# Performance work log

Measured on AMD Instinct MI355X. Metric: run time of the kernel, lower is better.

Reference implementation:

```python
import jax, jax.numpy as jnp
import numpy as np

B, N, D, L = 32, 1024, 128, 2  # batch graphs, nodes, hidden dim, num GIN layers
BN_EPS = 1e-5


def _batchnorm(x2d, gamma, beta):
    # Training-mode BatchNorm1d over flattened (B*N, D) with biased variance
    mean = jnp.mean(x2d, axis=0)
    var = jnp.mean(jnp.square(x2d - mean), axis=0)
    return (x2d - mean) * (gamma / jnp.sqrt(var + BN_EPS)) + beta


def setup_inputs() -> dict:
    key = jax.random.key(0)
    ks = jax.random.split(key, 12)
    s = 1.0 / np.sqrt(D)  # torch Linear default init scale
    inp = {
        "x": jax.random.normal(ks[0], (B, N, D), dtype=jnp.float32),
        "padded_nei": jax.random.randint(ks[1], (B, N, 8), 0, N, dtype=jnp.int64),
        "adj": jax.random.uniform(ks[2], (B, N, N), dtype=jnp.float32),
        # stacked per-layer params [L, ...]
        "W1": jax.random.uniform(ks[3], (L, D, D), jnp.float32, -s, s),
        "b1": jax.random.uniform(ks[4], (L, D), jnp.float32, -s, s),
        "W2": jax.random.uniform(ks[5], (L, D, D), jnp.float32, -s, s),
        "b2": jax.random.uniform(ks[6], (L, D), jnp.float32, -s, s),
        "g_in": jnp.ones((L, D), jnp.float32),   # MLP-internal BN gamma
        "be_in": jnp.zeros((L, D), jnp.float32),  # MLP-internal BN beta
        "g_out": jnp.ones((L, D), jnp.float32),  # GraphCNN outer BN gamma
        "be_out": jnp.zeros((L, D), jnp.float32),
    }
    return inp


def reference(x, padded_nei, adj, W1, b1, W2, b2, g_in, be_in, g_out, be_out):
    h = x  # [B, N, D]
    for l in range(L):
        # sum-pooling over neighbors via batched dense adjacency matmul
        pooled = jnp.einsum('bij,bjd->bid', adj, h)  # [B, N, D]
        # MLP: Linear -> BN -> ReLU -> Linear
        z = pooled @ W1[l] + b1[l]
        z = jax.nn.relu(_batchnorm(z.reshape(-1, D), g_in[l], be_in[l])).reshape(B, N, D)
        z = z @ W2[l] + b2[l]
        # outer BatchNorm1d + ReLU
        h = jax.nn.relu(_batchnorm(z.reshape(-1, D), g_out[l], be_out[l])).reshape(B, N, D)
    return h
```

## Files before the change

### kernel.cpp

```cpp
#include <hip/hip_runtime.h>
#include <stdint.h>


#define BB 32
#define NN 1024
#define DD 128
#define RR 32768

typedef __bf16 bf16_t;
typedef bf16_t bf16x8 __attribute__((ext_vector_type(8)));
typedef float f32x4 __attribute__((ext_vector_type(4)));

__device__ __forceinline__ unsigned short f2b(float f) {
  unsigned u = __float_as_uint(f);
  u += 0x7fff + ((u >> 16) & 1);
  return (unsigned short)(u >> 16);
}
__device__ __forceinline__ float b2f(unsigned short s) {
  return __uint_as_float((unsigned)s << 16);
}

__global__ __launch_bounds__(256) void k0_prep(const float* __restrict__ x,
                                               const float* __restrict__ W1,
                                               const float* __restrict__ W2,
                                               unsigned short* __restrict__ hT,
                                               unsigned short* __restrict__ W1T,
                                               unsigned short* __restrict__ W2T) {
  const int tid = threadIdx.x;
  if (blockIdx.x < 256) {
    const int b = blockIdx.x >> 3, nt = blockIdx.x & 7;
    __shared__ alignas(16) unsigned short T[128][136];
    const int r = tid >> 1, c0 = (tid & 1) * 64;
    const float* src = x + ((size_t)(b * 8 + nt) * 128 + r) * 128 + c0;
#pragma unroll
    for (int i = 0; i < 64; i += 4) {
      float4 v = *(const float4*)(src + i);
      int c = c0 + i;
      T[c][r] = f2b(v.x); T[c + 1][r] = f2b(v.y);
      T[c + 2][r] = f2b(v.z); T[c + 3][r] = f2b(v.w);
    }
    __syncthreads();
    const int d = tid >> 1, n0 = (tid & 1) * 64;
    unsigned short* dst = hT + ((size_t)b * DD + d) * NN + nt * 128 + n0;
#pragma unroll
    for (int i = 0; i < 64; i += 8)
      *(uint4*)(dst + i) = *(const uint4*)&T[d][n0 + i];
  } else {
    int idx = (blockIdx.x - 256) * 256 + tid;
    int w = idx >> 15;
    int rem = idx & 32767;
    int l = rem >> 14;
    int n = (rem >> 7) & 127;
    int k = rem & 127;
    const float* W = w ? W2 : W1;
    unsigned short* WT = w ? W2T : W1T;
    WT[((size_t)l * 128 + n) * 128 + k] = f2b(W[((size_t)l * 128 + k) * 128 + n]);
  }
}

__global__ __launch_bounds__(256, 2) void kA_pool_lin(
    const float* __restrict__ adj, const unsigned short* __restrict__ hT,
    const unsigned short* __restrict__ WT, const float* __restrict__ bias,
    unsigned short* __restrict__ z1b, float* __restrict__ gsum,
    float* __restrict__ gsq) {
  const int mt = blockIdx.x, b = blockIdx.y;
  const int tid = threadIdx.x;
  const int wave = tid >> 6, lane = tid & 63;
  const int wc = wave * 32;
  const int ln = lane & 15, q = lane >> 4;

  __shared__ union {
    struct {
      alignas(16) unsigned short As[64][72];
      alignas(16) unsigned short Bs[128][72];
    } p1;
    alignas(16) unsigned short As2[64][136];
  } sm;
  __shared__ alignas(16) unsigned short Ws[128][136];

#pragma unroll
  for (int p = 0; p < 8; p++) {
    int c = tid + p * 256;
    int n = c >> 4, k8 = (c & 15) * 8;
    *(uint4*)&Ws[n][k8] = *(const uint4*)&WT[n * 128 + k8];
  }

  const float* adjb = adj + ((size_t)b * NN + mt * 64) * NN;
  const unsigned short* hTb = hT + (size_t)b * DD * NN;

  f32x4 acc1[4][2];
  f32x4 zero = {0.f, 0.f, 0.f, 0.f};
#pragma unroll
  for (int i = 0; i < 4; i++) { acc1[i][0] = zero; acc1[i][1] = zero; }

  const int ar = tid >> 2, aseg = (tid & 3) * 16;
  const int br = tid >> 1, bh = (tid & 1) * 32;
  const float* pAsrc = adjb + (size_t)ar * NN + aseg;
  const unsigned short* pBsrc = hTb + (size_t)br * NN + bh;

  float4 pa[4];
  uint4 pb[4];
#pragma unroll
  for (int u = 0; u < 4; u++) {
    pa[u] = *(const float4*)(pAsrc + u * 4);
    pb[u] = *(const uint4*)(pBsrc + u * 8);
  }

  for (int k0 = 0; k0 < NN; k0 += 64) {
    __syncthreads();
    {
      alignas(16) unsigned short t[16];
#pragma unroll
      for (int u = 0; u < 4; u++) {
        t[u * 4] = f2b(pa[u].x); t[u * 4 + 1] = f2b(pa[u].y);
        t[u * 4 + 2] = f2b(pa[u].z); t[u * 4 + 3] = f2b(pa[u].w);
      }
      *(uint4*)&sm.p1.As[ar][aseg] = *(const uint4*)&t[0];
      *(uint4*)&sm.p1.As[ar][aseg + 8] = *(const uint4*)&t[8];
#pragma unroll
      for (int u = 0; u < 4; u++) *(uint4*)&sm.p1.Bs[br][bh + u * 8] = pb[u];
    }
    __syncthreads();
    if (k0 + 64 < NN) {
#pragma unroll
      for (int u = 0; u < 4; u++) {
        pa[u] = *(const float4*)(pAsrc + k0 + 64 + u * 4);
        pb[u] = *(const uint4*)(pBsrc + k0 + 64 + u * 8);
      }
    }
#pragma unroll
    for (int kk = 0; kk < 2; kk++) {
      bf16x8 af[4], bfr[2];
#pragma unroll
      for (int i = 0; i < 4; i++)
        af[i] = *(const bf16x8*)&sm.p1.As[i * 16 + ln][kk * 32 + q * 8];
#pragma unroll
      for (int j = 0; j < 2; j++)
        bfr[j] = *(const bf16x8*)&sm.p1.Bs[wc + j * 16 + ln][kk * 32 + q * 8];
#pragma unroll
      for (int i = 0; i < 4; i++)
#pragma unroll
        for (int j = 0; j < 2; j++)
          acc1[i][j] = __builtin_amdgcn_mfma_f32_16x16x32_bf16(af[i], bfr[j], acc1[i][j], 0, 0, 0);
    }
  }

  __syncthreads();
#pragma unroll
  for (int i = 0; i < 4; i++) {
    int row = i * 16 + q * 4;
#pragma unroll
    for (int j = 0; j < 2; j++) {
      int col = wc + j * 16 + ln;
#pragma unroll
      for (int r = 0; r < 4; r++) sm.As2[row + r][col] = f2b(acc1[i][j][r]);
    }
  }
  __syncthreads();

  f32x4 acc2[4][2];
#pragma unroll
  for (int i = 0; i < 4; i++) { acc2[i][0] = zero; acc2[i][1] = zero; }
#pragma unroll
  for (int ks = 0; ks < 4; ks++) {
    bf16x8 af[4], bfr[2];
#pragma unroll
    for (int i = 0; i < 4; i++)
      af[i] = *(const bf16x8*)&sm.As2[i * 16 + ln][ks * 32 + q * 8];
#pragma unroll
    for (int j = 0; j < 2; j++)
      bfr[j] = *(const bf16x8*)&Ws[wc + j * 16 + ln][ks * 32 + q * 8];
#pragma unroll
    for (int i = 0; i < 4; i++)
#pragma unroll
      for (int j = 0; j < 2; j++)
        acc2[i][j] = __builtin_amdgcn_mfma_f32_16x16x32_bf16(af[i], bfr[j], acc2[i][j], 0, 0, 0);
  }

  const size_t row0 = (size_t)b * NN + mt * 64;
#pragma unroll
  for (int j = 0; j < 2; j++) {
    int col = wc + j * 16 + ln;
    float bc = bias[col];
    float s1 = 0.f, s2 = 0.f;
#pragma unroll
    for (int i = 0; i < 4; i++) {
      int row = i * 16 + q * 4;
#pragma unroll
      for (int r = 0; r < 4; r++) {
        float v = acc2[i][j][r] + bc;
        z1b[(row0 + row + r) * 128 + col] = f2b(v);
        s1 += v; s2 += v * v;
      }
    }
    s1 += __shfl_xor(s1, 16); s1 += __shfl_xor(s1, 32);
    s2 += __shfl_xor(s2, 16); s2 += __shfl_xor(s2, 32);
    if (q == 0) { atomicAdd(&gsum[col], s1); atomicAdd(&gsq[col], s2); }
  }
}

__global__ __launch_bounds__(256, 2) void kB_lin(
    const unsigned short* __restrict__ Zin, const float* __restrict__ gsum_in,
    const float* __restrict__ gsq_in, const float* __restrict__ gamma,
    const float* __restrict__ beta, const unsigned short* __restrict__ WT,
    const float* __restrict__ bias, unsigned short* __restrict__ z2b,
    float* __restrict__ gsum, float* __restrict__ gsq) {
  const int mt = blockIdx.x;
  const int tid = threadIdx.x;
  const int wave = tid >> 6, lane = tid & 63;
  const int wc = wave * 32;
  const int ln = lane & 15, q = lane >> 4;

  __shared__ alignas(16) unsigned short Az[64][136];
  __shared__ alignas(16) unsigned short Ws[128][136];
  __shared__ float nsc[128], nsh[128];

  if (tid < 128) {
    float mean = gsum_in[tid] * (1.f / 32768.f);
    float var = gsq_in[tid] * (1.f / 32768.f) - mean * mean;
    float sc = gamma[tid] * rsqrtf(var + 1e-5f);
    nsc[tid] = sc; nsh[tid] = beta[tid] - mean * sc;
  }
#pragma unroll
  for (int p = 0; p < 8; p++) {
    int c = tid + p * 256;
    int n = c >> 4, k8 = (c & 15) * 8;
    *(uint4*)&Ws[n][k8] = *(const uint4*)&WT[n * 128 + k8];
  }
  __syncthreads();

  const size_t row0 = (size_t)mt * 64;
  {
    const int r = tid >> 2, c0 = (tid & 3) * 32;
    const unsigned short* src = Zin + (row0 + r) * 128 + c0;
#pragma unroll
    for (int u = 0; u < 4; u++) {
      uint4 raw = *(const uint4*)(src + u * 8);
      const unsigned short* s = (const unsigned short*)&raw;
      alignas(16) unsigned short t[8];
#pragma unroll
      for (int e = 0; e < 8; e++) {
        int c = c0 + u * 8 + e;
        t[e] = f2b(fmaxf(fmaf(b2f(s[e]), nsc[c], nsh[c]), 0.f));
      }
      *(uint4*)&Az[r][c0 + u * 8] = *(const uint4*)&t[0];
    }
  }
  __syncthreads();

  f32x4 acc[4][2];
  f32x4 zero = {0.f, 0.f, 0.f, 0.f};
#pragma unroll
  for (int i = 0; i < 4; i++) { acc[i][0] = zero; acc[i][1] = zero; }
#pragma unroll
  for (int ks = 0; ks < 4; ks++) {
    bf16x8 af[4], bfr[2];
#pragma unroll
    for (int i = 0; i < 4; i++)
      af[i] = *(const bf16x8*)&Az[i * 16 + ln][ks * 32 + q * 8];
#pragma unroll
    for (int j = 0; j < 2; j++)
      bfr[j] = *(const bf16x8*)&Ws[wc + j * 16 + ln][ks * 32 + q * 8];
#pragma unroll
    for (int i = 0; i < 4; i++)
#pragma unroll
      for (int j = 0; j < 2; j++)
        acc[i][j] = __builtin_amdgcn_mfma_f32_16x16x32_bf16(af[i], bfr[j], acc[i][j], 0, 0, 0);
  }

#pragma unroll
  for (int j = 0; j < 2; j++) {
    int col = wc + j * 16 + ln;
    float bc = bias[col];
    float s1 = 0.f, s2 = 0.f;
#pragma unroll
    for (int i = 0; i < 4; i++) {
      int row = i * 16 + q * 4;
#pragma unroll
      for (int r = 0; r < 4; r++) {
        float v = acc[i][j][r] + bc;
        z2b[(row0 + row + r) * 128 + col] = f2b(v);
        s1 += v; s2 += v * v;
      }
    }
    s1 += __shfl_xor(s1, 16); s1 += __shfl_xor(s1, 32);
    s2 += __shfl_xor(s2, 16); s2 += __shfl_xor(s2, 32);
    if (q == 0) { atomicAdd(&gsum[col], s1); atomicAdd(&gsq[col], s2); }
  }
}

__global__ __launch_bounds__(256) void k4_bnt(const unsigned short* __restrict__ Z,
                                              const float* __restrict__ gsum,
                                              const float* __restrict__ gsq,
                                              const float* __restrict__ gamma,
                                              const float* __restrict__ beta,
                                              unsigned short* __restrict__ hT) {
  const int b = blockIdx.x, nt = blockIdx.y, tid = threadIdx.x;
  __shared__ alignas(16) unsigned short T[128][136];
  __shared__ float nsc[128], nsh[128];
  if (tid < 128) {
    float mean = gsum[tid] * (1.f / 32768.f);
    float var = gsq[tid] * (1.f / 32768.f) - mean * mean;
    float sc = gamma[tid] * rsqrtf(var + 1e-5f);
    nsc[tid] = sc; nsh[tid] = beta[tid] - mean * sc;
  }
  __syncthreads();
  const int r = tid >> 1, c0 = (tid & 1) * 64;
  const unsigned short* src = Z + ((size_t)(b * 8 + nt) * 128 + r) * 128 + c0;
#pragma unroll
  for (int u = 0; u < 8; u++) {
    uint4 raw = *(const uint4*)(src + u * 8);
    const unsigned short* s = (const unsigned short*)&raw;
#pragma unroll
    for (int e = 0; e < 8; e++) {
      int c = c0 + u * 8 + e;
      T[c][r] = f2b(fmaxf(fmaf(b2f(s[e]), nsc[c], nsh[c]), 0.f));
    }
  }
  __syncthreads();
  const int d = tid >> 1, n0 = (tid & 1) * 64;
  unsigned short* dst = hT + ((size_t)b * DD + d) * NN + nt * 128 + n0;
#pragma unroll
  for (int i = 0; i < 64; i += 8)
    *(uint4*)(dst + i) = *(const uint4*)&T[d][n0 + i];
}

__global__ __launch_bounds__(256) void k4_out(const unsigned short* __restrict__ Z,
                                              const float* __restrict__ gsum,
                                              const float* __restrict__ gsq,
                                              const float* __restrict__ gamma,
                                              const float* __restrict__ beta,
                                              float* __restrict__ out) {
  const int blk = blockIdx.x, tid = threadIdx.x;
  __shared__ float nsc[128], nsh[128];
  if (tid < 128) {
    float mean = gsum[tid] * (1.f / 32768.f);
    float var = gsq[tid] * (1.f / 32768.f) - mean * mean;
    float sc = gamma[tid] * rsqrtf(var + 1e-5f);
    nsc[tid] = sc; nsh[tid] = beta[tid] - mean * sc;
  }
  __syncthreads();
  const int r = tid >> 1, c0 = (tid & 1) * 64;
  const unsigned short* src = Z + ((size_t)blk * 128 + r) * 128 + c0;
  float* dst = out + ((size_t)blk * 128 + r) * 128 + c0;
#pragma unroll
  for (int u = 0; u < 8; u++) {
    uint4 raw = *(const uint4*)(src + u * 8);
    const unsigned short* s = (const unsigned short*)&raw;
    float4 o;
    int c = c0 + u * 8;
    o.x = fmaxf(fmaf(b2f(s[0]), nsc[c], nsh[c]), 0.f);
    o.y = fmaxf(fmaf(b2f(s[1]), nsc[c + 1], nsh[c + 1]), 0.f);
    o.z = fmaxf(fmaf(b2f(s[2]), nsc[c + 2], nsh[c + 2]), 0.f);
    o.w = fmaxf(fmaf(b2f(s[3]), nsc[c + 3], nsh[c + 3]), 0.f);
    *(float4*)(dst + u * 8) = o;
    o.x = fmaxf(fmaf(b2f(s[4]), nsc[c + 4], nsh[c + 4]), 0.f);
    o.y = fmaxf(fmaf(b2f(s[5]), nsc[c + 5], nsh[c + 5]), 0.f);
    o.z = fmaxf(fmaf(b2f(s[6]), nsc[c + 6], nsh[c + 6]), 0.f);
    o.w = fmaxf(fmaf(b2f(s[7]), nsc[c + 7], nsh[c + 7]), 0.f);
    *(float4*)(dst + u * 8 + 4) = o;
  }
}

extern "C" void kernel_launch(void* const* d_in, const int* in_sizes, int n_in,
                              void* d_out, int out_size, void* d_ws, size_t ws_size,
                              hipStream_t stream) {
  const float* x = (const float*)d_in[0];
  const float* adj = (const float*)d_in[2];
  const float* W1 = (const float*)d_in[3];
  const float* b1 = (const float*)d_in[4];
  const float* W2 = (const float*)d_in[5];
  const float* b2 = (const float*)d_in[6];
  const float* g_in = (const float*)d_in[7];
  const float* be_in = (const float*)d_in[8];
  const float* g_out = (const float*)d_in[9];
  const float* be_out = (const float*)d_in[10];
  float* out = (float*)d_out;

  char* ws = (char*)d_ws;
  unsigned short* hT = (unsigned short*)ws;
  unsigned short* z1b = (unsigned short*)(ws + 8ull * 1024 * 1024);
  unsigned short* z2b = (unsigned short*)(ws + 16ull * 1024 * 1024);
  unsigned short* W1T = (unsigned short*)(ws + 24ull * 1024 * 1024);
  unsigned short* W2T = W1T + 2 * 128 * 128;
  float* stats = (float*)(ws + 25ull * 1024 * 1024);

  hipMemsetAsync(stats, 0, 4 * 256 * sizeof(float), stream);
  k0_prep<<<512, 256, 0, stream>>>(x, W1, W2, hT, W1T, W2T);

  for (int l = 0; l < 2; l++) {
    float* st_in = stats + (l * 2 + 0) * 256;
    float* st_out = stats + (l * 2 + 1) * 256;
    kA_pool_lin<<<dim3(16, 32), 256, 0, stream>>>(adj, hT, W1T + l * 16384,
                                                  b1 + l * 128, z1b, st_in,
                                                  st_in + 128);
    kB_lin<<<512, 256, 0, stream>>>(z1b, st_in, st_in + 128, g_in + l * 128,
                                    be_in + l * 128, W2T + l * 16384,
                                    b2 + l * 128, z2b, st_out, st_out + 128);
    if (l == 0)
      k4_bnt<<<dim3(32, 8), 256, 0, stream>>>(z2b, st_out, st_out + 128, g_out,
                                              be_out, hT);
    else
      k4_out<<<256, 256, 0, stream>>>(z2b, st_out, st_out + 128, g_out + 128,
                                      be_out + 128, out);
  }
}
```

Baseline: 371.7 us.

## Pre-convert adjacency to bf16 and stream tiles into LDS asynchronously

The prep kernel gains extra blocks that convert the fp32 adjacency to a bf16 copy in workspace. The pooling kernel then reads that copy. Its main loop is replaced by a double-buffered pipeline that loads tiles straight into LDS with global_load_lds, using an XOR-swizzled layout to avoid bank conflicts and explicit vmcnt waits plus barriers. The second linear layer's weight fragments move from LDS into registers. This aims to hide global load latency and remove the per-thread fp32-to-bf16 conversion in the hot loop, at the cost of an extra conversion pass over adjacency, a large added workspace buffer, and higher register use.

```diff
diff --git a/kernel.cpp b/kernel.cpp
--- a/kernel.cpp
+++ b/kernel.cpp
@@ -20,13 +20,29 @@
   return __uint_as_float((unsigned)s << 16);
 }
 
+#define GLL(GP, LP)                                              \
+  __builtin_amdgcn_global_load_lds(                              \
+      (const __attribute__((address_space(1))) void*)(GP),       \
+      (__attribute__((address_space(3))) void*)(LP), 16, 0, 0)
+
 __global__ __launch_bounds__(256) void k0_prep(const float* __restrict__ x,
+                                               const float* __restrict__ adj,
                                                const float* __restrict__ W1,
                                                const float* __restrict__ W2,
                                                unsigned short* __restrict__ hT,
                                                unsigned short* __restrict__ W1T,
-                                               unsigned short* __restrict__ W2T) {
+                                               unsigned short* __restrict__ W2T,
+                                               unsigned short* __restrict__ adjB) {
   const int tid = threadIdx.x;
+  if (blockIdx.x >= 512) {
+    size_t i8 = ((size_t)(blockIdx.x - 512) * 256 + tid) * 8;
+    float4 a = *(const float4*)(adj + i8);
+    float4 b = *(const float4*)(adj + i8 + 4);
+    alignas(16) unsigned short t[8] = {f2b(a.x), f2b(a.y), f2b(a.z), f2b(a.w),
+                                       f2b(b.x), f2b(b.y), f2b(b.z), f2b(b.w)};
+    *(uint4*)(adjB + i8) = *(const uint4*)t;
+    return;
+  }
   if (blockIdx.x < 256) {
     const int b = blockIdx.x >> 3, nt = blockIdx.x & 7;
     __shared__ alignas(16) unsigned short T[128][136];
@@ -59,7 +75,7 @@
 }
 
 __global__ __launch_bounds__(256, 2) void kA_pool_lin(
-    const float* __restrict__ adj, const unsigned short* __restrict__ hT,
+    const unsigned short* __restrict__ adjB, const unsigned short* __restrict__ hT,
     const unsigned short* __restrict__ WT, const float* __restrict__ bias,
     unsigned short* __restrict__ z1b, float* __restrict__ gsum,
     float* __restrict__ gsq) {
@@ -70,82 +86,83 @@
   const int ln = lane & 15, q = lane >> 4;
 
   __shared__ union {
-    struct {
-      alignas(16) unsigned short As[64][72];
-      alignas(16) unsigned short Bs[128][72];
-    } p1;
-    alignas(16) unsigned short As2[64][136];
+    unsigned short stage[2][12288];
+    unsigned short As2[64][136];
   } sm;
-  __shared__ alignas(16) unsigned short Ws[128][136];
-
-#pragma unroll
-  for (int p = 0; p < 8; p++) {
-    int c = tid + p * 256;
-    int n = c >> 4, k8 = (c & 15) * 8;
-    *(uint4*)&Ws[n][k8] = *(const uint4*)&WT[n * 128 + k8];
-  }
-
-  const float* adjb = adj + ((size_t)b * NN + mt * 64) * NN;
+
+  const unsigned short* adjb = adjB + ((size_t)b * NN + mt * 64) * NN;
   const unsigned short* hTb = hT + (size_t)b * DD * NN;
+
+  bf16x8 wfr[4][2];
+#pragma unroll
+  for (int ks = 0; ks < 4; ks++)
+#pragma unroll
+    for (int j = 0; j < 2; j++)
+      wfr[ks][j] = *(const bf16x8*)&WT[(size_t)(wc + j * 16 + ln) * 128 + ks * 32 + q * 8];
+  asm volatile("s_waitcnt vmcnt(0)" ::: "memory");
+
+  const int srow = tid >> 3;
+  const int sseg = (((tid & 7) ^ (srow & 7)) << 3);
+  const unsigned short* gA = adjb + (size_t)srow * NN + sseg;
+  const unsigned short* gB = hTb + (size_t)srow * NN + sseg;
+
+#define STAGE(P, K0)                                   \
+  do {                                                 \
+    unsigned short* dp = sm.stage[(P)];                \
+    GLL(gA + (K0), dp + tid * 8);                      \
+    GLL(gA + 32 * NN + (K0), dp + 2048 + tid * 8);     \
+    GLL(gB + (K0), dp + 4096 + tid * 8);               \
+    GLL(gB + 32 * NN + (K0), dp + 6144 + tid * 8);     \
+    GLL(gB + 64 * NN + (K0), dp + 8192 + tid * 8);     \
+    GLL(gB + 96 * NN + (K0), dp + 10240 + tid * 8);    \
+  } while (0)
+
+  STAGE(0, 0);
+  STAGE(1, 64);
 
   f32x4 acc1[4][2];
   f32x4 zero = {0.f, 0.f, 0.f, 0.f};
 #pragma unroll
   for (int i = 0; i < 4; i++) { acc1[i][0] = zero; acc1[i][1] = zero; }
 
-  const int ar = tid >> 2, aseg = (tid & 3) * 16;
-  const int br = tid >> 1, bh = (tid & 1) * 32;
-  const float* pAsrc = adjb + (size_t)ar * NN + aseg;
-  const unsigned short* pBsrc = hTb + (size_t)br * NN + bh;
-
-  float4 pa[4];
-  uint4 pb[4];
-#pragma unroll
-  for (int u = 0; u < 4; u++) {
-    pa[u] = *(const float4*)(pAsrc + u * 4);
-    pb[u] = *(const uint4*)(pBsrc + u * 8);
-  }
-
-  for (int k0 = 0; k0 < NN; k0 += 64) {
-    __syncthreads();
+  const int xorv = (ln & 7) << 4;
+
+#pragma unroll 2
+  for (int t = 0; t < 16; ++t) {
+    const int p = t & 1;
+    if (t < 15)
+      asm volatile("s_waitcnt vmcnt(6)" ::: "memory");
+    else
+      asm volatile("s_waitcnt vmcnt(0)" ::: "memory");
+    __builtin_amdgcn_s_barrier();
+    __builtin_amdgcn_sched_barrier(0);
     {
-      alignas(16) unsigned short t[16];
-#pragma unroll
-      for (int u = 0; u < 4; u++) {
-        t[u * 4] = f2b(pa[u].x); t[u * 4 + 1] = f2b(pa[u].y);
-        t[u * 4 + 2] = f2b(pa[u].z); t[u * 4 + 3] = f2b(pa[u].w);
+      const char* Ab = (const char*)sm.stage[p];
+      const char* Bb = Ab + 8192;
+#pragma unroll
+      for (int kk = 0; kk < 2; kk++) {
+        const int co = ((kk << 6) + (q << 4)) ^ xorv;
+        bf16x8 af[4], bfr[2];
+#pragma unroll
+        for (int i = 0; i < 4; i++)
+          af[i] = *(const bf16x8*)(Ab + (i * 16 + ln) * 128 + co);
+#pragma unroll
+        for (int j = 0; j < 2; j++)
+          bfr[j] = *(const bf16x8*)(Bb + (wc + j * 16 + ln) * 128 + co);
+#pragma unroll
+        for (int i = 0; i < 4; i++)
+#pragma unroll
+          for (int j = 0; j < 2; j++)
+            acc1[i][j] = __builtin_amdgcn_mfma_f32_16x16x32_bf16(af[i], bfr[j], acc1[i][j], 0, 0, 0);
       }
-      *(uint4*)&sm.p1.As[ar][aseg] = *(const uint4*)&t[0];
-      *(uint4*)&sm.p1.As[ar][aseg + 8] = *(const uint4*)&t[8];
-#pragma unroll
-      for (int u = 0; u < 4; u++) *(uint4*)&sm.p1.Bs[br][bh + u * 8] = pb[u];
-    }
-    __syncthreads();
-    if (k0 + 64 < NN) {
-#pragma unroll
-      for (int u = 0; u < 4; u++) {
-        pa[u] = *(const float4*)(pAsrc + k0 + 64 + u * 4);
-        pb[u] = *(const uint4*)(pBsrc + k0 + 64 + u * 8);
-      }
-    }
-#pragma unroll
-    for (int kk = 0; kk < 2; kk++) {
-      bf16x8 af[4], bfr[2];
-#pragma unroll
-      for (int i = 0; i < 4; i++)
-        af[i] = *(const bf16x8*)&sm.p1.As[i * 16 + ln][kk * 32 + q * 8];
-#pragma unroll
-      for (int j = 0; j < 2; j++)
-        bfr[j] = *(const bf16x8*)&sm.p1.Bs[wc + j * 16 + ln][kk * 32 + q * 8];
-#pragma unroll
-      for (int i = 0; i < 4; i++)
-#pragma unroll
-        for (int j = 0; j < 2; j++)
-          acc1[i][j] = __builtin_amdgcn_mfma_f32_16x16x32_bf16(af[i], bfr[j], acc1[i][j], 0, 0, 0);
-    }
-  }
-
-  __syncthreads();
+    }
+    __builtin_amdgcn_sched_barrier(0);
+    __builtin_amdgcn_s_barrier();
+    __builtin_amdgcn_sched_barrier(0);
+    if (t < 14) STAGE(p, (t + 2) * 64);
+  }
+#undef STAGE
+
 #pragma unroll
   for (int i = 0; i < 4; i++) {
     int row = i * 16 + q * 4;
@@ -163,18 +180,15 @@
   for (int i = 0; i < 4; i++) { acc2[i][0] = zero; acc2[i][1] = zero; }
 #pragma unroll
   for (int ks = 0; ks < 4; ks++) {
-    bf16x8 af[4], bfr[2];
+    bf16x8 af[4];
 #pragma unroll
     for (int i = 0; i < 4; i++)
       af[i] = *(const bf16x8*)&sm.As2[i * 16 + ln][ks * 32 + q * 8];
 #pragma unroll
-    for (int j = 0; j < 2; j++)
-      bfr[j] = *(const bf16x8*)&Ws[wc + j * 16 + ln][ks * 32 + q * 8];
-#pragma unroll
     for (int i = 0; i < 4; i++)
 #pragma unroll
       for (int j = 0; j < 2; j++)
-        acc2[i][j] = __builtin_amdgcn_mfma_f32_16x16x32_bf16(af[i], bfr[j], acc2[i][j], 0, 0, 0);
+        acc2[i][j] = __builtin_amdgcn_mfma_f32_16x16x32_bf16(af[i], wfr[ks][j], acc2[i][j], 0, 0, 0);
   }
 
   const size_t row0 = (size_t)b * NN + mt * 64;
@@ -384,14 +398,15 @@
   unsigned short* W1T = (unsigned short*)(ws + 24ull * 1024 * 1024);
   unsigned short* W2T = W1T + 2 * 128 * 128;
   float* stats = (float*)(ws + 25ull * 1024 * 1024);
+  unsigned short* adjB = (unsigned short*)(ws + 26ull * 1024 * 1024);
 
   hipMemsetAsync(stats, 0, 4 * 256 * sizeof(float), stream);
-  k0_prep<<<512, 256, 0, stream>>>(x, W1, W2, hT, W1T, W2T);
+  k0_prep<<<512 + 16384, 256, 0, stream>>>(x, adj, W1, W2, hT, W1T, W2T, adjB);
 
   for (int l = 0; l < 2; l++) {
     float* st_in = stats + (l * 2 + 0) * 256;
     float* st_out = stats + (l * 2 + 1) * 256;
-    kA_pool_lin<<<dim3(16, 32), 256, 0, stream>>>(adj, hT, W1T + l * 16384,
+    kA_pool_lin<<<dim3(16, 32), 256, 0, stream>>>(adjB, hT, W1T + l * 16384,
                                                   b1 + l * 128, z1b, st_in,
                                                   st_in + 128);
     kB_lin<<<512, 256, 0, stream>>>(z1b, st_in, st_in + 128, g_in + l * 128,
```

Result: faster. 348.8 us (-6.2%).
